# Performance work log

Hardware: AMD Instinct MI355X
Metric: run time of the kernel (lower is better)

The kernel has to match this reference:

```python
import jax, jax.numpy as jnp
import numpy as np

T, B, I, H, L, TAPE = 512, 1, 1024, 1024, 2, 30


def setup_inputs() -> dict:
    key = jax.random.key(0)
    ks = jax.random.split(key, 9)
    s = 1.0 / np.sqrt(H)  # pytorch LSTM default init scale
    u = lambda k, sh: jax.random.uniform(k, sh, jnp.float32, -s, s)
    return {
        "xs": jax.random.normal(ks[0], (T, B, I), jnp.float32),
        "w_ih": u(ks[1], (L, 4 * H, I)),
        "w_hh": u(ks[2], (L, 4 * H, H)),
        "b_ih": u(ks[3], (L, 4 * H)),
        "b_hh": u(ks[4], (L, 4 * H)),
        "attn_wh": jax.random.normal(ks[5], (L, H, H), jnp.float32),
        "attn_wx": jax.random.normal(ks[6], (L, H, I), jnp.float32),
        "attn_wht": jax.random.normal(ks[7], (L, H, H), jnp.float32),
        "attn_v": jax.random.normal(ks[8], (L, H), jnp.float32),
    }


def _lstm_step(x, h_prev, c_prev, w_ih, w_hh, b_ih, b_hh):
    # x: (B, I); h_prev, c_prev: (L, B, H). PyTorch gate order i,f,g,o. No dropout (eval/deterministic).
    inp = x
    hs, cs = [], []
    for l in range(L):
        g = inp @ w_ih[l].T + b_ih[l] + h_prev[l] @ w_hh[l].T + b_hh[l]
        i_g, f_g, g_g, o_g = jnp.split(g, 4, axis=-1)
        c = jax.nn.sigmoid(f_g) * c_prev[l] + jax.nn.sigmoid(i_g) * jnp.tanh(g_g)
        h = jax.nn.sigmoid(o_g) * jnp.tanh(c)
        hs.append(h)
        cs.append(c)
        inp = h
    return jnp.stack(hs), jnp.stack(cs)  # (L, B, H) each


def _forward(xs, w_ih, w_hh, b_ih, b_hh, attn_wh, attn_wx, attn_wht, attn_v):
    zeros_state = jnp.zeros((L, B, H), xs.dtype)

    # Phase 1: prev_hidden/cell tapes are never updated in the first loop, so each of the
    # first TAPE steps runs the LSTM from a zero state -> fully parallel via vmap.
    p1 = lambda x: _lstm_step(x, zeros_state, zeros_state, w_ih, w_hh, b_ih, b_hh)
    h1, c1 = jax.vmap(p1)(xs[:TAPE])  # (TAPE, L, B, H)
    h_tape = jax.lax.stop_gradient(h1)  # .detach() in the original
    c_tape = jax.lax.stop_gradient(c1)

    cum = jnp.zeros((T, H), xs.dtype)
    cum = cum.at[:TAPE].set(h1[:, -1, 0, :])  # hidden_state[-1].squeeze(), B==1

    # einsum('jll,...') / einsum('ijj,...') only use the diagonals of attn_wh / attn_wht
    diag_wh = jnp.diagonal(attn_wh, axis1=1, axis2=2)    # (L, H)
    diag_wht = jnp.diagonal(attn_wht, axis1=1, axis2=2)  # (L, H)

    def step(carry, x):
        h_tape, c_tape, prev_h = carry
        hidden_attn = diag_wh[None, :, None, :] * h_tape          # (TAPE, L, B, H)
        x_attn = jnp.einsum('lhi,bi->lbh', attn_wx, x)            # (L, B, H)
        ht_attn = diag_wht[:, None, :] * prev_h                   # (L, B, H)
        a = jnp.tanh(hidden_attn + (x_attn + ht_attn)[None])      # (TAPE, L, B, H)
        scores = jnp.einsum('tlbh,lh->tlb', a, attn_v)            # (TAPE, L, B)
        alpha = jax.nn.softmax(scores, axis=0)                    # softmax over tape dim
        new_h = jnp.einsum('tlb,tlbh->lbh', alpha, h_tape)
        new_c = jnp.einsum('tlb,tlbh->lbh', alpha, c_tape)
        h, c = _lstm_step(x, new_h, new_c, w_ih, w_hh, b_ih, b_hh)
        h_tape = jnp.concatenate([h_tape[1:], h[None]], axis=0)   # tape shift
        c_tape = jnp.concatenate([c_tape[1:], c[None]], axis=0)
        return (h_tape, c_tape, new_h), h[-1, 0, :]

    _, ys = jax.lax.scan(step, (h_tape, c_tape, zeros_state), xs[TAPE:])
    # second loop indexes cum from 0, overwriting the phase-1 entries (faithful to source)
    cum = cum.at[: T - TAPE].set(ys)
    return cum


def reference(xs, w_ih, w_hh, b_ih, b_hh, attn_wh, attn_wx, attn_wht, attn_v):
    return _forward(xs, w_ih, w_hh, b_ih, b_hh, attn_wh, attn_wx, attn_wht, attn_v)
```

## Files before the change

kernel.cpp:

```cpp
#include <hip/hip_runtime.h>
#include <math.h>

#define LSTRIDE 4194304

__device__ __forceinline__ float fast_tanh(float x) {
  x = fminf(9.f, fmaxf(-9.f, x));
  float e = __expf(2.f * x);
  return (e - 1.f) * __builtin_amdgcn_rcpf(e + 1.f);
}
__device__ __forceinline__ float fsig(float x) {
  return __builtin_amdgcn_rcpf(1.f + __expf(-x));
}
__device__ __forceinline__ float sigp(float x) { return 1.0f / (1.0f + expf(-x)); }

__device__ __forceinline__ float cload(const float* p) {
  return __hip_atomic_load(p, __ATOMIC_RELAXED, __HIP_MEMORY_SCOPE_AGENT);
}
__device__ __forceinline__ void cstore(float* p, float v) {
  __hip_atomic_store(p, v, __ATOMIC_RELAXED, __HIP_MEMORY_SCOPE_AGENT);
}
__device__ __forceinline__ float2 cload2(const float* p) {
  unsigned long long v = __hip_atomic_load((const unsigned long long*)p,
                                           __ATOMIC_RELAXED, __HIP_MEMORY_SCOPE_AGENT);
  float2 r;
  r.x = __uint_as_float((unsigned)v);
  r.y = __uint_as_float((unsigned)(v >> 32));
  return r;
}

__global__ __launch_bounds__(256) void gemm_nt(
    const float* __restrict__ A, const float* __restrict__ X, float* __restrict__ Out,
    const float* __restrict__ b1, const float* __restrict__ b2,
    int M, int ldx, int ldo)
{
  __shared__ float As[64][65];
  __shared__ float Xs[64][65];
  const int tid = threadIdx.x;
  const int tn = tid & 15, tm = tid >> 4;
  const int bn = blockIdx.x * 64, bm = blockIdx.y * 64;
  float acc[4][4];
  #pragma unroll
  for (int i = 0; i < 4; ++i)
    #pragma unroll
    for (int j = 0; j < 4; ++j) acc[i][j] = 0.f;

  for (int k0 = 0; k0 < 1024; k0 += 64) {
    #pragma unroll
    for (int r = 0; r < 4; ++r) {
      int linear = r * 1024 + tid * 4;
      int nn = linear >> 6, kk = linear & 63;
      float4 av = *(const float4*)(A + (size_t)(bn + nn) * 1024 + k0 + kk);
      As[nn][kk+0] = av.x; As[nn][kk+1] = av.y; As[nn][kk+2] = av.z; As[nn][kk+3] = av.w;
      float4 xv = make_float4(0.f, 0.f, 0.f, 0.f);
      if (bm + nn < M) xv = *(const float4*)(X + (size_t)(bm + nn) * ldx + k0 + kk);
      Xs[nn][kk+0] = xv.x; Xs[nn][kk+1] = xv.y; Xs[nn][kk+2] = xv.z; Xs[nn][kk+3] = xv.w;
    }
    __syncthreads();
    #pragma unroll 16
    for (int kk = 0; kk < 64; ++kk) {
      float av[4], xv[4];
      #pragma unroll
      for (int u = 0; u < 4; ++u) { av[u] = As[tn*4+u][kk]; xv[u] = Xs[tm*4+u][kk]; }
      #pragma unroll
      for (int i = 0; i < 4; ++i)
        #pragma unroll
        for (int j = 0; j < 4; ++j) acc[i][j] += xv[i] * av[j];
    }
    __syncthreads();
  }
  #pragma unroll
  for (int i = 0; i < 4; ++i) {
    int m = bm + tm * 4 + i;
    if (m >= M) continue;
    #pragma unroll
    for (int j = 0; j < 4; ++j) {
      int n = bn + tn * 4 + j;
      float r = acc[i][j];
      if (b1) r += b1[n];
      if (b2) r += b2[n];
      Out[(size_t)m * ldo + n] = r;
    }
  }
}

__global__ void diag_k(const float* __restrict__ wh, const float* __restrict__ wht,
                       float* __restrict__ diag)
{
  int i = blockIdx.x * 256 + threadIdx.x;
  if (i < 2048) {
    int l = i >> 10, h = i & 1023;
    size_t idx = (size_t)l * 1048576 + (size_t)h * 1025;
    diag[i]        = wh[idx];
    diag[2048 + i] = wht[idx];
  }
}

__global__ __launch_bounds__(256) void phase1_l0_k(const float* __restrict__ XI0,
    float* __restrict__ tapeh, float* __restrict__ tapec, float* __restrict__ h0p1)
{
  int t = blockIdx.x;
  #pragma unroll
  for (int r = 0; r < 4; ++r) {
    int c = threadIdx.x + r * 256;
    float gi = XI0[t*4096 + c];
    float gg = XI0[t*4096 + 2048 + c];
    float go = XI0[t*4096 + 3072 + c];
    float cc = sigp(gi) * tanhf(gg);
    float hh = sigp(go) * tanhf(cc);
    tapeh[t*2048 + c] = hh;
    tapec[t*2048 + c] = cc;
    h0p1[t*1024 + c] = hh;
  }
}

__global__ __launch_bounds__(256) void phase1_l1_k(const float* __restrict__ G1,
    float* __restrict__ tapeh, float* __restrict__ tapec)
{
  int t = blockIdx.x;
  #pragma unroll
  for (int r = 0; r < 4; ++r) {
    int c = threadIdx.x + r * 256;
    float gi = G1[t*4096 + c];
    float gg = G1[t*4096 + 2048 + c];
    float go = G1[t*4096 + 3072 + c];
    float cc = sigp(gi) * tanhf(gg);
    float hh = sigp(go) * tanhf(cc);
    tapeh[t*2048 + 1024 + c] = hh;
    tapec[t*2048 + 1024 + c] = cc;
  }
}

__device__ __forceinline__ float red16(float p) {
  #pragma unroll
  for (int o = 8; o >= 1; o >>= 1) p += __shfl_xor(p, o, 16);
  return p;
}

__device__ __forceinline__ void arrive(unsigned* __restrict__ base, int gw) {
  asm volatile("s_waitcnt vmcnt(0)" ::: "memory");
  __syncthreads();
  if (threadIdx.x == 0) {
    unsigned o = __hip_atomic_fetch_add(&base[(gw >> 4) * 16], 1u,
                                        __ATOMIC_RELAXED, __HIP_MEMORY_SCOPE_AGENT);
    if (((o + 1) & 15u) == 0u)
      __hip_atomic_fetch_add(&base[128], 1u,
                             __ATOMIC_RELAXED, __HIP_MEMORY_SCOPE_AGENT);
  }
}

__device__ __forceinline__ void waitf(const unsigned* __restrict__ fOwn, unsigned tOwn,
                                      const unsigned* __restrict__ fOth, unsigned tOth) {
  if (threadIdx.x < 2) {
    const unsigned* fp = threadIdx.x ? fOth : fOwn;
    unsigned tgt = threadIdx.x ? tOth : tOwn;
    if (tgt) {
      while (__hip_atomic_load(fp, __ATOMIC_RELAXED, __HIP_MEMORY_SCOPE_AGENT) < tgt)
        __builtin_amdgcn_s_sleep(1);
    }
  }
  __syncthreads();
  asm volatile("" ::: "memory");
}

template <int LW>
__device__ __forceinline__ void run_group(
    const int gw,
    const float* __restrict__ wih, const float* __restrict__ whh,
    const float* __restrict__ bih, const float* __restrict__ bhh,
    const float* __restrict__ diag, const float* __restrict__ av,
    const float* __restrict__ XI0, const float* __restrict__ XA,
    const float* __restrict__ tapehG, const float* __restrict__ tapecG,
    const float* __restrict__ Pg,
    float* __restrict__ scoresG, float* __restrict__ prevh,
    float* __restrict__ h0cur, float* __restrict__ h1cur,
    float* __restrict__ outp, unsigned* __restrict__ bar,
    float* tape, float* hA, float* hB, float* Pl, float* tc,
    float* sc2, float* aw, float* gls, float* ihs, float* ncs,
    float* bsum, float* sred)
{
  const int tid = threadIdx.x;
  const int rid = tid >> 4, sub = tid & 15;
  const int row = ((rid >> 3) << 10) + (gw << 3) + (rid & 7);
  const bool isScore = (gw < 58);
  const int ii = gw >> 1, half = gw & 1;
  const int d = (half << 9) + tid;
  const int h2 = tid * 2;

  unsigned* __restrict__ barOwn = bar + (LW ? 256 : 0);
  const unsigned* __restrict__ fOwn = barOwn + 128;
  const unsigned* __restrict__ fOth = bar + (LW ? 0 : 256) + 128;

  float wA[64];
  float wB[LW ? 64 : 1];
  {
    const float* pa = whh + (size_t)LW * LSTRIDE + (size_t)row * 1024 + sub * 64;
    #pragma unroll
    for (int i = 0; i < 16; ++i) {
      float4 v = ((const float4*)pa)[i];
      wA[4*i] = v.x; wA[4*i+1] = v.y; wA[4*i+2] = v.z; wA[4*i+3] = v.w;
    }
    if (LW) {
      const float* pb = wih + LSTRIDE + (size_t)row * 1024 + sub * 64;
      #pragma unroll
      for (int i = 0; i < 16; ++i) {
        float4 v = ((const float4*)pb)[i];
        wB[4*i] = v.x; wB[4*i+1] = v.y; wB[4*i+2] = v.z; wB[4*i+3] = v.w;
      }
    }
  }
  if (LW && sub == 0) bsum[rid] = bih[4096 + row] + bhh[4096 + row];
  for (int k = tid; k < 960; k += 512) {
    int s = k >> 5, r = k & 31;
    int rr = ((r >> 3) << 10) + (gw << 3) + (r & 7);
    Pl[s * 34 + r] = Pg[s * 4096 + rr];
  }
  for (int k = tid; k < 240; k += 512) {
    int s = k >> 3, c = k & 7;
    tc[s * 9 + c] = tapecG[s * 2048 + LW * 1024 + (gw << 3) + c];
  }
  if (isScore) {
    for (int k = tid; k < 3840; k += 512) {
      int s = k >> 7, off = (k & 127) << 2;
      *(float4*)&tape[s * 512 + off] =
          *(const float4*)&tapehG[s * 2048 + LW * 1024 + (half << 9) + off];
    }
  }
  const float ddx = diag[LW*1024 + h2],        ddy = diag[LW*1024 + h2 + 1];
  const float ttx = diag[2048 + LW*1024 + h2], tty = diag[2048 + LW*1024 + h2 + 1];
  const float vvx = av[LW*1024 + h2],          vvy = av[LW*1024 + h2 + 1];
  const float ddT = diag[LW*1024 + d];
  const float ttT = diag[2048 + LW*1024 + d];
  const float vvT = av[LW*1024 + d];
  __syncthreads();

  if (isScore) {
    for (int s = ii; s < 30; s += 29) {
      float xa = XA[(size_t)30 * 2048 + LW * 1024 + d];
      float part = vvT * fast_tanh(ddT * tape[s * 512 + tid] + xa);
      #pragma unroll
      for (int o = 32; o >= 1; o >>= 1) part += __shfl_xor(part, o, 64);
      if ((tid & 63) == 0) sred[tid >> 6] = part;
      __syncthreads();
      if (tid == 0) {
        float tot = 0.f;
        #pragma unroll
        for (int i = 0; i < 8; ++i) tot += sred[i];
        cstore(&scoresG[LW * 64 + s * 2 + half], tot);
      }
      __syncthreads();
    }
  }
  arrive(barOwn, gw);

  for (int t = 30; t < 512; ++t) {
    float2 xan = make_float2(0.f, 0.f);
    if (t > 30) xan = *(const float2*)&XA[(size_t)t * 2048 + LW * 1024 + h2];
    float xi = 0.f;
    if (LW == 0 && sub == 0) xi = XI0[(size_t)t * 4096 + row];
    float xaT = 0.f;
    if (isScore && t < 511) xaT = XA[(size_t)(t + 1) * 2048 + LW * 1024 + d];

    unsigned tOwn = 8u * (unsigned)(t - 29);
    unsigned tOth;
    if (LW == 0)
      tOth = (t >= 34) ? 8u * (unsigned)(t - 32) : 0u;
    else
      tOth = 8u * (unsigned)(t - 28);
    waitf(fOwn, tOwn, fOth, tOth);

    const int tmod = t % 30;
    const int pslot = (tmod == 0) ? 29 : tmod - 1;

    if (tid < 60) sc2[tid] = cload(&scoresG[(t & 1) * 128 + LW * 64 + tid]);
    float2 hva = make_float2(0.f, 0.f), hvb = make_float2(0.f, 0.f),
           ph = make_float2(0.f, 0.f);
    if (LW == 0) {
      if (t > 30) hva = cload2(&h0cur[(size_t)((t - 1) & 3) * 1024 + h2]);
    } else {
      hva = cload2(&h0cur[(size_t)(t & 3) * 1024 + h2]);
      if (t > 30) hvb = cload2(&h1cur[((t - 1) & 1) * 1024 + h2]);
    }
    if (t > 30) ph = cload2(&prevh[((t - 1) & 1) * 2048 + LW * 1024 + h2]);
    {
      int o = (h2 >> 6) * 66 + (h2 & 63);
      if (LW || t > 30) { hA[o] = hva.x; hA[o + 1] = hva.y; }
      if (LW && t > 30) { hB[o] = hvb.x; hB[o + 1] = hvb.y; }
    }
    __syncthreads();

    if (t > 30) {
      float2 hn = LW ? hvb : hva;
      float np = vvx * fast_tanh(ddx * hn.x + xan.x + ttx * ph.x)
               + vvy * fast_tanh(ddy * hn.y + xan.y + tty * ph.y);
      #pragma unroll
      for (int o = 32; o >= 1; o >>= 1) np += __shfl_xor(np, o, 64);
      if ((tid & 63) == 0) sred[tid >> 6] = np;
      if (isScore) {
        int loc = h2 - (half << 9);
        if ((unsigned)loc < 512u) {
          tape[pslot * 512 + loc]     = hn.x;
          tape[pslot * 512 + loc + 1] = hn.y;
        }
      }
      const float* hp = LW ? hB : hA;
      float pc = 0.f;
      #pragma unroll
      for (int i = 0; i < 64; ++i) pc += wA[i] * hp[sub * 66 + i];
      pc = red16(pc);
      if (sub == 0) Pl[pslot * 34 + rid] = pc;
    }
    if (LW) {
      float ih = 0.f;
      #pragma unroll
      for (int i = 0; i < 64; ++i) ih += wB[i] * hA[sub * 66 + i];
      ih = red16(ih);
      if (sub == 0) ihs[rid] = ih + bsum[rid];
    }
    __syncthreads();

    if (tid < 32) {
      float npv = 0.f;
      if (t > 30) {
        float x = (tid < 8) ? sred[tid] : 0.f;
        #pragma unroll
        for (int o = 4; o >= 1; o >>= 1) x += __shfl_xor(x, o, 8);
        npv = __shfl(x, 0, 32);
      }
      float v = (tid < 30) ? sc2[2 * tid] + sc2[2 * tid + 1] : -1e30f;
      if (t > 30 && tid == pslot) v = npv;
      float m = v;
      #pragma unroll
      for (int o = 16; o >= 1; o >>= 1) m = fmaxf(m, __shfl_xor(m, o, 32));
      float e = (tid < 30) ? __expf(v - m) : 0.f;
      float sm = e;
      #pragma unroll
      for (int o = 16; o >= 1; o >>= 1) sm += __shfl_xor(sm, o, 32);
      aw[tid] = e * __builtin_amdgcn_rcpf(sm);
    }
    __syncthreads();

    {
      float p = aw[sub] * Pl[sub * 34 + rid];
      if (sub < 14) p += aw[sub + 16] * Pl[(sub + 16) * 34 + rid];
      p = red16(p);
      if (sub == 0) gls[rid] = p + (LW ? ihs[rid] : xi);
      if (rid < 8) {
        float pn = aw[sub] * tc[sub * 9 + rid];
        if (sub < 14) pn += aw[sub + 16] * tc[(sub + 16) * 9 + rid];
        pn = red16(pn);
        if (sub == 0) ncs[rid] = pn;
      }
    }
    __syncthreads();

    if (tid < 8) {
      float gi = gls[tid], gf = gls[8 + tid], gg = gls[16 + tid], go = gls[24 + tid];
      float cv = fsig(gf) * ncs[tid] + fsig(gi) * fast_tanh(gg);
      float hv = fsig(go) * fast_tanh(cv);
      if (LW == 0) {
        cstore(&h0cur[(size_t)(t & 3) * 1024 + (gw << 3) + tid], hv);
      } else {
        outp[(size_t)(t - 30) * 1024 + (gw << 3) + tid] = hv;
        cstore(&h1cur[(t & 1) * 1024 + (gw << 3) + tid], hv);
      }
      tc[tmod * 9 + tid] = cv;
    }

    if (isScore && t < 511) {
      int ss = tmod + 1 + ii; if (ss >= 30) ss -= 30;
      float acc = 0.f;
      #pragma unroll
      for (int s = 0; s < 30; ++s) acc += aw[s] * tape[s * 512 + tid];
      if (ii == 0) cstore(&prevh[(t & 1) * 2048 + LW * 1024 + d], acc);
      float part = vvT * fast_tanh(ddT * tape[ss * 512 + tid] + xaT + ttT * acc);
      #pragma unroll
      for (int o = 32; o >= 1; o >>= 1) part += __shfl_xor(part, o, 64);
      if ((tid & 63) == 0) sred[tid >> 6] = part;
      __syncthreads();
      if (tid == 0) {
        float tot = 0.f;
        #pragma unroll
        for (int i = 0; i < 8; ++i) tot += sred[i];
        cstore(&scoresG[((t + 1) & 1) * 128 + LW * 64 + ss * 2 + half], tot);
      }
    }

    arrive(barOwn, gw);
  }
}

__global__ __launch_bounds__(512, 2) void scan_fused(
    const float* __restrict__ wih, const float* __restrict__ whh,
    const float* __restrict__ bih, const float* __restrict__ bhh,
    const float* __restrict__ diag, const float* __restrict__ av,
    const float* __restrict__ XI0, const float* __restrict__ XA,
    const float* __restrict__ tapehG, const float* __restrict__ tapecG,
    const float* __restrict__ P0g, const float* __restrict__ P1g,
    float* __restrict__ scoresG, float* __restrict__ prevh,
    float* __restrict__ h0cur, float* __restrict__ h1cur,
    float* __restrict__ outp, unsigned* __restrict__ bar)
{
  __shared__ float tape[30 * 512];
  __shared__ float hA[16 * 66], hB[16 * 66];
  __shared__ float Pl[30 * 34];
  __shared__ float tc[30 * 9];
  __shared__ float sc2[64], aw[32], gls[32], ihs[32], ncs[8], bsum[32], sred[8];
  if (blockIdx.x < 128)
    run_group<0>(blockIdx.x, wih, whh, bih, bhh, diag, av, XI0, XA, tapehG, tapecG,
                 P0g, scoresG, prevh, h0cur, h1cur, outp, bar,
                 tape, hA, hB, Pl, tc, sc2, aw, gls, ihs, ncs, bsum, sred);
  else
    run_group<1>(blockIdx.x - 128, wih, whh, bih, bhh, diag, av, XI0, XA, tapehG, tapecG,
                 P1g, scoresG, prevh, h0cur, h1cur, outp, bar,
                 tape, hA, hB, Pl, tc, sc2, aw, gls, ihs, ncs, bsum, sred);
}

extern "C" void kernel_launch(void* const* d_in, const int* in_sizes, int n_in,
                              void* d_out, int out_size, void* d_ws, size_t ws_size,
                              hipStream_t stream) {
  (void)in_sizes; (void)n_in; (void)out_size; (void)ws_size;
  const float* xs    = (const float*)d_in[0];
  const float* w_ih  = (const float*)d_in[1];
  const float* w_hh  = (const float*)d_in[2];
  const float* b_ih  = (const float*)d_in[3];
  const float* b_hh  = (const float*)d_in[4];
  const float* a_wh  = (const float*)d_in[5];
  const float* a_wx  = (const float*)d_in[6];
  const float* a_wht = (const float*)d_in[7];
  const float* a_v   = (const float*)d_in[8];
  float* outp = (float*)d_out;

  float* ws     = (float*)d_ws;
  float* XI0    = ws;
  float* XA     = XI0    + 512 * 4096;
  float* tapehG = XA     + 512 * 2048;
  float* tapecG = tapehG + 30 * 2048;
  float* P0g    = tapecG + 30 * 2048;
  float* P1g    = P0g    + 30 * 4096;
  float* diag   = P1g    + 30 * 4096;
  float* scor   = diag   + 4096;
  float* prevh  = scor   + 256;
  float* h0cur  = prevh  + 4096;
  float* h1cur  = h0cur  + 4096;
  float* h0p1   = h1cur  + 2048;
  float* G1b    = h0p1   + 30 * 1024;
  unsigned* bar = (unsigned*)(G1b + 30 * 4096);

  hipMemsetAsync(outp + (size_t)482 * 1024, 0, 30 * 1024 * sizeof(float), stream);
  hipMemsetAsync(bar, 0, 2048, stream);

  diag_k<<<8, 256, 0, stream>>>(a_wh, a_wht, diag);

  gemm_nt<<<dim3(64, 8), 256, 0, stream>>>(w_ih, xs, XI0, b_ih, b_hh, 512, 1024, 4096);
  gemm_nt<<<dim3(16, 8), 256, 0, stream>>>(a_wx, xs, XA, nullptr, nullptr, 512, 1024, 2048);
  gemm_nt<<<dim3(16, 8), 256, 0, stream>>>(a_wx + LSTRIDE / 4, xs, XA + 1024, nullptr, nullptr, 512, 1024, 2048);

  phase1_l0_k<<<30, 256, 0, stream>>>(XI0, tapehG, tapecG, h0p1);
  gemm_nt<<<dim3(64, 1), 256, 0, stream>>>(w_ih + LSTRIDE, h0p1, G1b, b_ih + 4096, b_hh + 4096, 30, 1024, 4096);
  phase1_l1_k<<<30, 256, 0, stream>>>(G1b, tapehG, tapecG);

  gemm_nt<<<dim3(64, 1), 256, 0, stream>>>(w_hh, tapehG, P0g, nullptr, nullptr, 30, 2048, 4096);
  gemm_nt<<<dim3(64, 1), 256, 0, stream>>>(w_hh + LSTRIDE, tapehG + 1024, P1g, nullptr, nullptr, 30, 2048, 4096);

  const float* wihp = w_ih;
  const float* whhp = w_hh;
  const float* bihp = b_ih;
  const float* bhhp = b_hh;
  void* kargs[] = {
    (void*)&wihp, (void*)&whhp, (void*)&bihp, (void*)&bhhp,
    (void*)&diag, (void*)&a_v,  (void*)&XI0,  (void*)&XA,
    (void*)&tapehG, (void*)&tapecG, (void*)&P0g, (void*)&P1g,
    (void*)&scor, (void*)&prevh, (void*)&h0cur, (void*)&h1cur,
    (void*)&outp, (void*)&bar
  };
  hipLaunchCooperativeKernel((void*)scan_fused, dim3(256), dim3(512), kargs, 0, stream);
}
```

Measured before the change: 3.543 ms.

## Compute newest-slot attention score partials in the owning block instead of broadcasting prev_h

Each block now keeps its own 8-element slice of the h tape and computes the attention-score term for the newest tape slot right after producing h. It publishes one partial per block to a small global buffer (npG). This replaces the old path, which wrote the full attention-weighted prev_h vector globally and had every block recompute the new-slot score with a block-wide reduction and an extra __syncthreads. The step-critical path loses a full-vector global read, a reduction and a barrier, at the cost of a 64-lane cross-block partial sum and a small extra weighted sum per block.

Result: slower. 3.633 ms (+2.5%).

```diff
diff --git a/kernel.cpp b/kernel.cpp
--- a/kernel.cpp
+++ b/kernel.cpp
@@ -171,11 +171,11 @@
     const float* __restrict__ XI0, const float* __restrict__ XA,
     const float* __restrict__ tapehG, const float* __restrict__ tapecG,
     const float* __restrict__ Pg,
-    float* __restrict__ scoresG, float* __restrict__ prevh,
+    float* __restrict__ scoresG, float* __restrict__ npG,
     float* __restrict__ h0cur, float* __restrict__ h1cur,
     float* __restrict__ outp, unsigned* __restrict__ bar,
-    float* tape, float* hA, float* hB, float* Pl, float* tc,
-    float* sc2, float* aw, float* gls, float* ihs, float* ncs,
+    float* tape, float* hA, float* hB, float* Pl, float* tc, float* tape8,
+    float* aw, float* gls, float* ihs, float* ncs,
     float* bsum, float* sred)
 {
   const int tid = threadIdx.x;
@@ -217,6 +217,7 @@
   for (int k = tid; k < 240; k += 512) {
     int s = k >> 3, c = k & 7;
     tc[s * 9 + c] = tapecG[s * 2048 + LW * 1024 + (gw << 3) + c];
+    tape8[s * 8 + c] = tapehG[s * 2048 + LW * 1024 + (gw << 3) + c];
   }
   if (isScore) {
     for (int k = tid; k < 3840; k += 512) {
@@ -225,9 +226,11 @@
           *(const float4*)&tapehG[s * 2048 + LW * 1024 + (half << 9) + off];
     }
   }
-  const float ddx = diag[LW*1024 + h2],        ddy = diag[LW*1024 + h2 + 1];
-  const float ttx = diag[2048 + LW*1024 + h2], tty = diag[2048 + LW*1024 + h2 + 1];
-  const float vvx = av[LW*1024 + h2],          vvy = av[LW*1024 + h2 + 1];
+  float d8 = 0.f, t8 = 0.f, v8 = 0.f;
+  if (tid < 8) {
+    int dd = LW * 1024 + (gw << 3) + tid;
+    d8 = diag[dd]; t8 = diag[2048 + dd]; v8 = av[dd];
+  }
   const float ddT = diag[LW*1024 + d];
   const float ttT = diag[2048 + LW*1024 + d];
   const float vvT = av[LW*1024 + d];
@@ -245,7 +248,7 @@
         float tot = 0.f;
         #pragma unroll
         for (int i = 0; i < 8; ++i) tot += sred[i];
-        cstore(&scoresG[LW * 64 + s * 2 + half], tot);
+        cstore(&scoresG[LW * 64 + 2 * s + half], tot);
       }
       __syncthreads();
     }
@@ -253,10 +256,13 @@
   arrive(barOwn, gw);
 
   for (int t = 30; t < 512; ++t) {
-    float2 xan = make_float2(0.f, 0.f);
-    if (t > 30) xan = *(const float2*)&XA[(size_t)t * 2048 + LW * 1024 + h2];
+    const int tmod = t % 30;
+    const int pslot = (tmod == 0) ? 29 : tmod - 1;
     float xi = 0.f;
     if (LW == 0 && sub == 0) xi = XI0[(size_t)t * 4096 + row];
+    float xa8 = 0.f;
+    if (tid < 8 && t < 511)
+      xa8 = XA[(size_t)(t + 1) * 2048 + LW * 1024 + (gw << 3) + tid];
     float xaT = 0.f;
     if (isScore && t < 511) xaT = XA[(size_t)(t + 1) * 2048 + LW * 1024 + d];
 
@@ -268,19 +274,16 @@
       tOth = 8u * (unsigned)(t - 28);
     waitf(fOwn, tOwn, fOth, tOth);
 
-    const int tmod = t % 30;
-    const int pslot = (tmod == 0) ? 29 : tmod - 1;
-
-    if (tid < 60) sc2[tid] = cload(&scoresG[(t & 1) * 128 + LW * 64 + tid]);
-    float2 hva = make_float2(0.f, 0.f), hvb = make_float2(0.f, 0.f),
-           ph = make_float2(0.f, 0.f);
+    float2 hva = make_float2(0.f, 0.f), hvb = make_float2(0.f, 0.f);
     if (LW == 0) {
       if (t > 30) hva = cload2(&h0cur[(size_t)((t - 1) & 3) * 1024 + h2]);
     } else {
       hva = cload2(&h0cur[(size_t)(t & 3) * 1024 + h2]);
       if (t > 30) hvb = cload2(&h1cur[((t - 1) & 1) * 1024 + h2]);
     }
-    if (t > 30) ph = cload2(&prevh[((t - 1) & 1) * 2048 + LW * 1024 + h2]);
+    float2 s2 = make_float2(0.f, 0.f), np2 = make_float2(0.f, 0.f);
+    if (tid < 30) s2 = cload2(&scoresG[(t & 1) * 128 + LW * 64 + 2 * tid]);
+    if (tid < 64 && t > 30) np2 = cload2(&npG[(t & 1) * 256 + LW * 128 + 2 * tid]);
     {
       int o = (h2 >> 6) * 66 + (h2 & 63);
       if (LW || t > 30) { hA[o] = hva.x; hA[o + 1] = hva.y; }
@@ -290,11 +293,6 @@
 
     if (t > 30) {
       float2 hn = LW ? hvb : hva;
-      float np = vvx * fast_tanh(ddx * hn.x + xan.x + ttx * ph.x)
-               + vvy * fast_tanh(ddy * hn.y + xan.y + tty * ph.y);
-      #pragma unroll
-      for (int o = 32; o >= 1; o >>= 1) np += __shfl_xor(np, o, 64);
-      if ((tid & 63) == 0) sred[tid >> 6] = np;
       if (isScore) {
         int loc = h2 - (half << 9);
         if ((unsigned)loc < 512u) {
@@ -316,26 +314,23 @@
       ih = red16(ih);
       if (sub == 0) ihs[rid] = ih + bsum[rid];
     }
-    __syncthreads();
-
-    if (tid < 32) {
-      float npv = 0.f;
+    if (tid < 64) {
+      float np = 0.f;
       if (t > 30) {
-        float x = (tid < 8) ? sred[tid] : 0.f;
-        #pragma unroll
-        for (int o = 4; o >= 1; o >>= 1) x += __shfl_xor(x, o, 8);
-        npv = __shfl(x, 0, 32);
-      }
-      float v = (tid < 30) ? sc2[2 * tid] + sc2[2 * tid + 1] : -1e30f;
-      if (t > 30 && tid == pslot) v = npv;
+        np = np2.x + np2.y;
+        #pragma unroll
+        for (int o = 32; o >= 1; o >>= 1) np += __shfl_xor(np, o, 64);
+      }
+      float v = (tid < 30) ? s2.x + s2.y : -1e30f;
+      if (t > 30 && tid == pslot) v = np;
       float m = v;
       #pragma unroll
-      for (int o = 16; o >= 1; o >>= 1) m = fmaxf(m, __shfl_xor(m, o, 32));
+      for (int o = 32; o >= 1; o >>= 1) m = fmaxf(m, __shfl_xor(m, o, 64));
       float e = (tid < 30) ? __expf(v - m) : 0.f;
       float sm = e;
       #pragma unroll
-      for (int o = 16; o >= 1; o >>= 1) sm += __shfl_xor(sm, o, 32);
-      aw[tid] = e * __builtin_amdgcn_rcpf(sm);
+      for (int o = 32; o >= 1; o >>= 1) sm += __shfl_xor(sm, o, 64);
+      if (tid < 32) aw[tid] = e * __builtin_amdgcn_rcpf(sm);
     }
     __syncthreads();
 
@@ -364,6 +359,16 @@
         cstore(&h1cur[(t & 1) * 1024 + (gw << 3) + tid], hv);
       }
       tc[tmod * 9 + tid] = cv;
+      if (t < 511) {
+        float pv = 0.f;
+        #pragma unroll
+        for (int s = 0; s < 30; ++s) pv += aw[s] * tape8[s * 8 + tid];
+        float term = v8 * fast_tanh(d8 * hv + xa8 + t8 * pv);
+        tape8[tmod * 8 + tid] = hv;
+        #pragma unroll
+        for (int o = 4; o >= 1; o >>= 1) term += __shfl_xor(term, o, 8);
+        if (tid == 0) cstore(&npG[((t + 1) & 1) * 256 + LW * 128 + gw], term);
+      }
     }
 
     if (isScore && t < 511) {
@@ -371,7 +376,6 @@
       float acc = 0.f;
       #pragma unroll
       for (int s = 0; s < 30; ++s) acc += aw[s] * tape[s * 512 + tid];
-      if (ii == 0) cstore(&prevh[(t & 1) * 2048 + LW * 1024 + d], acc);
       float part = vvT * fast_tanh(ddT * tape[ss * 512 + tid] + xaT + ttT * acc);
       #pragma unroll
       for (int o = 32; o >= 1; o >>= 1) part += __shfl_xor(part, o, 64);
@@ -381,7 +385,7 @@
         float tot = 0.f;
         #pragma unroll
         for (int i = 0; i < 8; ++i) tot += sred[i];
-        cstore(&scoresG[((t + 1) & 1) * 128 + LW * 64 + ss * 2 + half], tot);
+        cstore(&scoresG[((t + 1) & 1) * 128 + LW * 64 + 2 * ss + half], tot);
       }
     }
 
@@ -396,7 +400,7 @@
     const float* __restrict__ XI0, const float* __restrict__ XA,
     const float* __restrict__ tapehG, const float* __restrict__ tapecG,
     const float* __restrict__ P0g, const float* __restrict__ P1g,
-    float* __restrict__ scoresG, float* __restrict__ prevh,
+    float* __restrict__ scoresG, float* __restrict__ npG,
     float* __restrict__ h0cur, float* __restrict__ h1cur,
     float* __restrict__ outp, unsigned* __restrict__ bar)
 {
@@ -404,15 +408,16 @@
   __shared__ float hA[16 * 66], hB[16 * 66];
   __shared__ float Pl[30 * 34];
   __shared__ float tc[30 * 9];
-  __shared__ float sc2[64], aw[32], gls[32], ihs[32], ncs[8], bsum[32], sred[8];
+  __shared__ float tape8[30 * 8];
+  __shared__ float aw[32], gls[32], ihs[32], ncs[8], bsum[32], sred[8];
   if (blockIdx.x < 128)
     run_group<0>(blockIdx.x, wih, whh, bih, bhh, diag, av, XI0, XA, tapehG, tapecG,
-                 P0g, scoresG, prevh, h0cur, h1cur, outp, bar,
-                 tape, hA, hB, Pl, tc, sc2, aw, gls, ihs, ncs, bsum, sred);
+                 P0g, scoresG, npG, h0cur, h1cur, outp, bar,
+                 tape, hA, hB, Pl, tc, tape8, aw, gls, ihs, ncs, bsum, sred);
   else
     run_group<1>(blockIdx.x - 128, wih, whh, bih, bhh, diag, av, XI0, XA, tapehG, tapecG,
-                 P1g, scoresG, prevh, h0cur, h1cur, outp, bar,
-                 tape, hA, hB, Pl, tc, sc2, aw, gls, ihs, ncs, bsum, sred);
+                 P1g, scoresG, npG, h0cur, h1cur, outp, bar,
+                 tape, hA, hB, Pl, tc, tape8, aw, gls, ihs, ncs, bsum, sred);
 }
 
 extern "C" void kernel_launch(void* const* d_in, const int* in_sizes, int n_in,
@@ -439,8 +444,8 @@
   float* P1g    = P0g    + 30 * 4096;
   float* diag   = P1g    + 30 * 4096;
   float* scor   = diag   + 4096;
-  float* prevh  = scor   + 256;
-  float* h0cur  = prevh  + 4096;
+  float* npG    = scor   + 256;
+  float* h0cur  = npG    + 512;
   float* h1cur  = h0cur  + 4096;
   float* h0p1   = h1cur  + 2048;
   float* G1b    = h0p1   + 30 * 1024;
@@ -470,7 +475,7 @@
     (void*)&wihp, (void*)&whhp, (void*)&bihp, (void*)&bhhp,
     (void*)&diag, (void*)&a_v,  (void*)&XI0,  (void*)&XA,
     (void*)&tapehG, (void*)&tapecG, (void*)&P0g, (void*)&P1g,
-    (void*)&scor, (void*)&prevh, (void*)&h0cur, (void*)&h1cur,
+    (void*)&scor, (void*)&npG, (void*)&h0cur, (void*)&h1cur,
     (void*)&outp, (void*)&bar
   };
   hipLaunchCooperativeKernel((void*)scan_fused, dim3(256), dim3(512), kargs, 0, stream);
```
